# Kernel optimization log

Hardware: AMD Instinct MI355X
Metric: run time of the kernel (lower is better)

Reference implementation:

```python
import math
import jax, jax.numpy as jnp
import numpy as np

S = 4096          # total packed tokens (b*s with bsz=1)
NUM_HEADS = 16
HEAD_DIM = 80
SCALE = 1.0 / math.sqrt(HEAD_DIM)


def setup_inputs() -> dict:
    key = jax.random.key(0)
    kq, kk, kv = jax.random.split(key, 3)
    q = jax.random.normal(kq, (S, NUM_HEADS, HEAD_DIM), dtype=jnp.float32)
    k = jax.random.normal(kk, (S, NUM_HEADS, HEAD_DIM), dtype=jnp.float32)
    v = jax.random.normal(kv, (S, NUM_HEADS, HEAD_DIM), dtype=jnp.float32)
    # 4 packed sequences of 1024 tokens each (flatten_batch=True, bsz=1)
    cu_seqlens = jnp.array([0, 1024, 2048, 3072, 4096], dtype=jnp.int32)
    return {"q": q, "k": k, "v": v, "bsz": 1, "cu_seqlens": cu_seqlens}


def reference(q, k, v, bsz, cu_seqlens):
    # q/k/v: [(b s), h, d]; flatten_batch=True so bsz == 1
    s = q.shape[0] // bsz
    h, d = q.shape[1], q.shape[2]

    # Block-diagonal mask from cu_seqlens: True inside each packed sequence.
    seg = jnp.searchsorted(cu_seqlens[1:], jnp.arange(s), side="right")  # [s]
    mask = seg[:, None] == seg[None, :]                                  # [s, s]

    # '(b s) h d -> b h s d'
    qb = q.reshape(bsz, s, h, d).transpose(0, 2, 1, 3)
    kb = k.reshape(bsz, s, h, d).transpose(0, 2, 1, 3)
    vb = v.reshape(bsz, s, h, d).transpose(0, 2, 1, 3)

    scores = jnp.einsum("bhsd,bhtd->bhst", qb, kb) * SCALE
    bias = jnp.where(mask, jnp.zeros((), scores.dtype), jnp.finfo(scores.dtype).min)
    attn = jax.nn.softmax((scores + bias).astype(jnp.float32), axis=-1).astype(q.dtype)

    out = jnp.einsum("bhst,bhtd->bhsd", attn, vb)
    # 'b h s d -> (b s) h d'
    return out.transpose(0, 2, 1, 3).reshape(bsz * s, h, d)
```

## Files before the change

kernel.cpp:

```cpp
#include <hip/hip_runtime.h>
#include <hip/hip_bf16.h>
#include <math.h>

#define NTOK 4096
#define NH 16
#define HD 80
#define TOKSTRIDE (NH * HD)
#define QBLK 64
#define KVBLK 64
#define KSTR 80
#define VSTR 72
#define PSTR 72

typedef __bf16 bf16x4 __attribute__((ext_vector_type(4)));
typedef __bf16 bf16x8 __attribute__((ext_vector_type(8)));
typedef float  f32x4  __attribute__((ext_vector_type(4)));

__global__ __launch_bounds__(256)
void prepack(const float* __restrict__ qg, const float* __restrict__ kg,
             const float* __restrict__ vg, __bf16* __restrict__ qb,
             __bf16* __restrict__ kb, __bf16* __restrict__ vtb) {
  __shared__ __align__(16) __bf16 Vl[HD][VSTR];
  const int tid  = threadIdx.x;
  const int tok0 = blockIdx.x * 64;
  const int h    = blockIdx.y;
  const float qscale = 1.4426950408889634f / sqrtf((float)HD);

  for (int i = tid; i < 64 * 20; i += 256) {
    const int row = i / 20;
    const int c4  = (i % 20) * 4;
    const size_t gsrc = (size_t)(tok0 + row) * TOKSTRIDE + h * HD + c4;
    const size_t gdst = ((size_t)h * NTOK + tok0 + row) * HD + c4;

    float4 fq = *reinterpret_cast<const float4*>(qg + gsrc);
    bf16x4 uq;
    uq[0] = (__bf16)(fq.x * qscale); uq[1] = (__bf16)(fq.y * qscale);
    uq[2] = (__bf16)(fq.z * qscale); uq[3] = (__bf16)(fq.w * qscale);
    *reinterpret_cast<bf16x4*>(qb + gdst) = uq;

    float4 fk = *reinterpret_cast<const float4*>(kg + gsrc);
    bf16x4 uk;
    uk[0] = (__bf16)fk.x; uk[1] = (__bf16)fk.y;
    uk[2] = (__bf16)fk.z; uk[3] = (__bf16)fk.w;
    *reinterpret_cast<bf16x4*>(kb + gdst) = uk;

    float4 fv = *reinterpret_cast<const float4*>(vg + gsrc);
    Vl[c4 + 0][row] = (__bf16)fv.x; Vl[c4 + 1][row] = (__bf16)fv.y;
    Vl[c4 + 2][row] = (__bf16)fv.z; Vl[c4 + 3][row] = (__bf16)fv.w;
  }
  __syncthreads();
  for (int i = tid; i < HD * 8; i += 256) {
    const int d  = i / 8;
    const int c8 = (i % 8) * 8;
    bf16x8 val = *reinterpret_cast<const bf16x8*>(&Vl[d][c8]);
    *reinterpret_cast<bf16x8*>(vtb + ((size_t)h * HD + d) * NTOK + tok0 + c8) = val;
  }
}

__global__ __launch_bounds__(256, 4)
void vis_attn5(const __bf16* __restrict__ qb, const __bf16* __restrict__ kb,
               const __bf16* __restrict__ vtb, const int* __restrict__ cu,
               int n_cu, float* __restrict__ outg) {
  __shared__ __align__(16) __bf16 Kl[(KVBLK + 1) * KSTR];
  __shared__ __align__(16) __bf16 Vt[HD][VSTR];
  __shared__ __align__(16) __bf16 Pl[QBLK][PSTR];

  const int tid  = threadIdx.x;
  const int w    = tid >> 6;
  const int lane = tid & 63;
  const int lr   = lane & 15;
  const int g    = lane >> 4;

  const int q0 = blockIdx.x * QBLK;
  const int h  = blockIdx.y;

  int kv_start = 0, kv_end = NTOK;
  for (int i = 0; i + 1 < n_cu; ++i) {
    int a = cu[i], b = cu[i + 1];
    if (q0 >= a && q0 < b) { kv_start = a; kv_end = b; }
  }

  if (tid < 16) Kl[KVBLK * KSTR + tid] = (__bf16)0.0f;

  const int qrow = q0 + w * 16 + lr;
  const __bf16* qrptr = qb + ((size_t)h * NTOK + qrow) * HD;
  bf16x8 qf[3];
  #pragma unroll
  for (int c = 0; c < 3; ++c) {
    const int dbase = c * 32 + g * 8;
    if (dbase < HD) {
      qf[c] = *reinterpret_cast<const bf16x8*>(qrptr + dbase);
    } else {
      #pragma unroll
      for (int j = 0; j < 8; ++j) qf[c][j] = (__bf16)0.0f;
    }
  }

  bf16x8 vfl;
  {
    const __bf16 o = (lr == 0) ? (__bf16)1.0f : (__bf16)0.0f;
    #pragma unroll
    for (int j = 0; j < 8; ++j) vfl[j] = o;
  }

  f32x4 O[6];
  #pragma unroll
  for (int n = 0; n < 6; ++n) O[n] = (f32x4){0.f, 0.f, 0.f, 0.f};

  bf16x8 st[5];
  const __bf16* kbh  = kb  + (size_t)h * NTOK * HD;
  const __bf16* vtbh = vtb + (size_t)h * HD * NTOK;

  {
    const int kv0 = kv_start;
    #pragma unroll
    for (int j = 0; j < 5; ++j) {
      const int c = tid + j * 256;
      if (c < 640) {
        const int row = c / 10, col = (c % 10) * 8;
        st[j] = *reinterpret_cast<const bf16x8*>(kbh + (size_t)(kv0 + row) * HD + col);
      } else {
        const int c2 = c - 640, d = c2 / 8, kc = (c2 % 8) * 8;
        st[j] = *reinterpret_cast<const bf16x8*>(vtbh + (size_t)d * NTOK + kv0 + kc);
      }
    }
  }

  for (int kv0 = kv_start; kv0 < kv_end; kv0 += KVBLK) {
    __syncthreads();
    #pragma unroll
    for (int j = 0; j < 5; ++j) {
      const int c = tid + j * 256;
      if (c < 640) {
        const int row = c / 10, col = (c % 10) * 8;
        *reinterpret_cast<bf16x8*>(&Kl[row * KSTR + col]) = st[j];
      } else {
        const int c2 = c - 640, d = c2 / 8, kc = (c2 % 8) * 8;
        *reinterpret_cast<bf16x8*>(&Vt[d][kc]) = st[j];
      }
    }
    __syncthreads();

    if (kv0 + KVBLK < kv_end) {
      const int kvn = kv0 + KVBLK;
      #pragma unroll
      for (int j = 0; j < 5; ++j) {
        const int c = tid + j * 256;
        if (c < 640) {
          const int row = c / 10, col = (c % 10) * 8;
          st[j] = *reinterpret_cast<const bf16x8*>(kbh + (size_t)(kvn + row) * HD + col);
        } else {
          const int c2 = c - 640, d = c2 / 8, kc = (c2 % 8) * 8;
          st[j] = *reinterpret_cast<const bf16x8*>(vtbh + (size_t)d * NTOK + kvn + kc);
        }
      }
    }

    f32x4 S[4];
    __builtin_amdgcn_s_setprio(1);
    #pragma unroll
    for (int t = 0; t < 4; ++t) {
      S[t] = (f32x4){0.f, 0.f, 0.f, 0.f};
      #pragma unroll
      for (int c = 0; c < 3; ++c) {
        bf16x8 kf = *reinterpret_cast<const bf16x8*>(&Kl[(t * 16 + lr) * KSTR + c * 32 + g * 8]);
        S[t] = __builtin_amdgcn_mfma_f32_16x16x32_bf16(qf[c], kf, S[t], 0, 0, 0);
      }
    }
    __builtin_amdgcn_s_setprio(0);

    #pragma unroll
    for (int t = 0; t < 4; ++t) {
      #pragma unroll
      for (int r = 0; r < 4; ++r)
        S[t][r] = exp2f(S[t][r]);
    }

    #pragma unroll
    for (int t = 0; t < 4; ++t) {
      #pragma unroll
      for (int r = 0; r < 4; ++r)
        Pl[w * 16 + g * 4 + r][t * 16 + lr] = (__bf16)S[t][r];
    }

    #pragma unroll
    for (int kc = 0; kc < 2; ++kc) {
      bf16x8 pf = *reinterpret_cast<const bf16x8*>(&Pl[w * 16 + lr][kc * 32 + g * 8]);
      __builtin_amdgcn_s_setprio(1);
      #pragma unroll
      for (int n = 0; n < 5; ++n) {
        bf16x8 vf = *reinterpret_cast<const bf16x8*>(&Vt[n * 16 + lr][kc * 32 + g * 8]);
        O[n] = __builtin_amdgcn_mfma_f32_16x16x32_bf16(pf, vf, O[n], 0, 0, 0);
      }
      O[5] = __builtin_amdgcn_mfma_f32_16x16x32_bf16(pf, vfl, O[5], 0, 0, 0);
      __builtin_amdgcn_s_setprio(0);
    }
  }

  float inv[4];
  #pragma unroll
  for (int r = 0; r < 4; ++r) {
    float l = __shfl(O[5][r], lane & 48);
    inv[r] = 1.0f / l;
  }
  const int orow0 = q0 + w * 16 + g * 4;
  #pragma unroll
  for (int n = 0; n < 5; ++n) {
    #pragma unroll
    for (int r = 0; r < 4; ++r)
      outg[(size_t)(orow0 + r) * TOKSTRIDE + h * HD + n * 16 + lr] = O[n][r] * inv[r];
  }
}

__global__ __launch_bounds__(256, 4)
void vis_attn_fb(const float* __restrict__ qg, const float* __restrict__ kg,
                 const float* __restrict__ vg, const int* __restrict__ cu,
                 int n_cu, float* __restrict__ outg) {
  __shared__ __align__(16) __bf16 Kl[KVBLK][104];
  __shared__ __align__(16) __bf16 Vt[HD][72];
  __shared__ __align__(16) __bf16 Pl[64][72];

  const int tid  = threadIdx.x;
  const int w    = tid >> 6;
  const int lane = tid & 63;
  const int lr   = lane & 15;
  const int g    = lane >> 4;
  const int q0 = blockIdx.x * 64;
  const int h  = blockIdx.y;

  int kv_start = 0, kv_end = NTOK;
  for (int i = 0; i + 1 < n_cu; ++i) {
    int a = cu[i], b = cu[i + 1];
    if (q0 >= a && q0 < b) { kv_start = a; kv_end = b; }
  }
  for (int i = tid; i < KVBLK * 16; i += 256)
    Kl[i >> 4][HD + (i & 15)] = (__bf16)0.0f;

  const float qscale = 1.4426950408889634f / sqrtf((float)HD);
  const int qrow = q0 + w * 16 + lr;
  const float* qptr = qg + (size_t)qrow * TOKSTRIDE + h * HD;
  bf16x8 qf[3];
  #pragma unroll
  for (int c = 0; c < 3; ++c) {
    const int dbase = c * 32 + g * 8;
    if (dbase < HD) {
      float4 f0 = *reinterpret_cast<const float4*>(qptr + dbase);
      float4 f1 = *reinterpret_cast<const float4*>(qptr + dbase + 4);
      qf[c][0] = (__bf16)(f0.x * qscale); qf[c][1] = (__bf16)(f0.y * qscale);
      qf[c][2] = (__bf16)(f0.z * qscale); qf[c][3] = (__bf16)(f0.w * qscale);
      qf[c][4] = (__bf16)(f1.x * qscale); qf[c][5] = (__bf16)(f1.y * qscale);
      qf[c][6] = (__bf16)(f1.z * qscale); qf[c][7] = (__bf16)(f1.w * qscale);
    } else {
      #pragma unroll
      for (int j = 0; j < 8; ++j) qf[c][j] = (__bf16)0.0f;
    }
  }

  f32x4 O[5];
  #pragma unroll
  for (int n = 0; n < 5; ++n) O[n] = (f32x4){0.f, 0.f, 0.f, 0.f};
  float m_run[4] = {-1e30f, -1e30f, -1e30f, -1e30f};
  float l_run[4] = {0.f, 0.f, 0.f, 0.f};

  for (int kv0 = kv_start; kv0 < kv_end; kv0 += KVBLK) {
    __syncthreads();
    for (int i = tid; i < KVBLK * (HD / 4); i += 256) {
      const int row = i / (HD / 4);
      const int c4  = (i % (HD / 4)) * 4;
      float4 f = *reinterpret_cast<const float4*>(
          kg + (size_t)(kv0 + row) * TOKSTRIDE + h * HD + c4);
      Kl[row][c4 + 0] = (__bf16)f.x; Kl[row][c4 + 1] = (__bf16)f.y;
      Kl[row][c4 + 2] = (__bf16)f.z; Kl[row][c4 + 3] = (__bf16)f.w;
    }
    for (int i = tid; i < KVBLK * (HD / 4); i += 256) {
      const int row = i / (HD / 4);
      const int c4  = (i % (HD / 4)) * 4;
      float4 f = *reinterpret_cast<const float4*>(
          vg + (size_t)(kv0 + row) * TOKSTRIDE + h * HD + c4);
      Vt[c4 + 0][row] = (__bf16)f.x; Vt[c4 + 1][row] = (__bf16)f.y;
      Vt[c4 + 2][row] = (__bf16)f.z; Vt[c4 + 3][row] = (__bf16)f.w;
    }
    __syncthreads();

    f32x4 S[4];
    #pragma unroll
    for (int t = 0; t < 4; ++t) {
      S[t] = (f32x4){0.f, 0.f, 0.f, 0.f};
      #pragma unroll
      for (int c = 0; c < 3; ++c) {
        bf16x8 kf = *reinterpret_cast<const bf16x8*>(&Kl[t * 16 + lr][c * 32 + g * 8]);
        S[t] = __builtin_amdgcn_mfma_f32_16x16x32_bf16(qf[c], kf, S[t], 0, 0, 0);
      }
    }
    float pmax[4];
    #pragma unroll
    for (int r = 0; r < 4; ++r)
      pmax[r] = fmaxf(fmaxf(S[0][r], S[1][r]), fmaxf(S[2][r], S[3][r]));
    #pragma unroll
    for (int r = 0; r < 4; ++r) {
      pmax[r] = fmaxf(pmax[r], __shfl_xor(pmax[r], 1));
      pmax[r] = fmaxf(pmax[r], __shfl_xor(pmax[r], 2));
      pmax[r] = fmaxf(pmax[r], __shfl_xor(pmax[r], 4));
      pmax[r] = fmaxf(pmax[r], __shfl_xor(pmax[r], 8));
    }
    float alpha[4];
    #pragma unroll
    for (int r = 0; r < 4; ++r) {
      float mn = fmaxf(m_run[r], pmax[r]);
      alpha[r] = exp2f(m_run[r] - mn);
      m_run[r] = mn;
    }
    #pragma unroll
    for (int t = 0; t < 4; ++t) {
      #pragma unroll
      for (int r = 0; r < 4; ++r)
        S[t][r] = exp2f(S[t][r] - m_run[r]);
    }
    float rsum[4];
    #pragma unroll
    for (int r = 0; r < 4; ++r) {
      rsum[r] = (S[0][r] + S[1][r]) + (S[2][r] + S[3][r]);
      rsum[r] += __shfl_xor(rsum[r], 1);
      rsum[r] += __shfl_xor(rsum[r], 2);
      rsum[r] += __shfl_xor(rsum[r], 4);
      rsum[r] += __shfl_xor(rsum[r], 8);
      l_run[r] = l_run[r] * alpha[r] + rsum[r];
    }
    #pragma unroll
    for (int n = 0; n < 5; ++n) {
      #pragma unroll
      for (int r = 0; r < 4; ++r) O[n][r] *= alpha[r];
    }
    #pragma unroll
    for (int t = 0; t < 4; ++t) {
      #pragma unroll
      for (int r = 0; r < 4; ++r)
        Pl[w * 16 + g * 4 + r][t * 16 + lr] = (__bf16)S[t][r];
    }
    #pragma unroll
    for (int kc = 0; kc < 2; ++kc) {
      bf16x8 pf = *reinterpret_cast<const bf16x8*>(&Pl[w * 16 + lr][kc * 32 + g * 8]);
      #pragma unroll
      for (int n = 0; n < 5; ++n) {
        bf16x8 vf = *reinterpret_cast<const bf16x8*>(&Vt[n * 16 + lr][kc * 32 + g * 8]);
        O[n] = __builtin_amdgcn_mfma_f32_16x16x32_bf16(pf, vf, O[n], 0, 0, 0);
      }
    }
  }

  float inv[4];
  #pragma unroll
  for (int r = 0; r < 4; ++r) inv[r] = 1.0f / l_run[r];
  const int orow0 = q0 + w * 16 + g * 4;
  #pragma unroll
  for (int n = 0; n < 5; ++n) {
    #pragma unroll
    for (int r = 0; r < 4; ++r)
      outg[(size_t)(orow0 + r) * TOKSTRIDE + h * HD + n * 16 + lr] = O[n][r] * inv[r];
  }
}

extern "C" void kernel_launch(void* const* d_in, const int* in_sizes, int n_in,
                              void* d_out, int out_size, void* d_ws, size_t ws_size,
                              hipStream_t stream) {
  const float* q  = (const float*)d_in[0];
  const float* k  = (const float*)d_in[1];
  const float* v  = (const float*)d_in[2];
  const int* cu   = (const int*)d_in[4];
  const int n_cu  = in_sizes[4];
  float* out      = (float*)d_out;

  const size_t one = (size_t)NH * NTOK * HD * sizeof(__bf16);

  if (ws_size >= 3 * one) {
    __bf16* qb  = (__bf16*)d_ws;
    __bf16* kb  = (__bf16*)((char*)d_ws + one);
    __bf16* vtb = (__bf16*)((char*)d_ws + 2 * one);
    dim3 gp(NTOK / 64, NH);
    prepack<<<gp, 256, 0, stream>>>(q, k, v, qb, kb, vtb);
    dim3 ga(NTOK / QBLK, NH);
    vis_attn5<<<ga, 256, 0, stream>>>(qb, kb, vtb, cu, n_cu, out);
  } else {
    dim3 gf(NTOK / 64, NH);
    vis_attn_fb<<<gf, 256, 0, stream>>>(q, k, v, cu, n_cu, out);
  }
}
```

Baseline: 64.26 us.

## Split attention waves 2x2 over query rows and KV columns with LDS reduction

Reorganizes the four waves from one 16-row query strip each into a 2x2 grid: each wave handles 32 query rows against half of the 64-key block. Each K and V fragment read from LDS now feeds two MFMAs, which is meant to cut LDS read traffic per MFMA. Because each wave only sees half the keys, the partial O and row-sum accumulators are combined at the end through an LDS buffer that aliases the K/V/P shared memory. The price is extra registers for two query tiles and a final cross-wave reduction with additional barriers.

```diff
diff --git a/kernel.cpp b/kernel.cpp
--- a/kernel.cpp
+++ b/kernel.cpp
@@ -58,15 +58,19 @@
 }
 
 __global__ __launch_bounds__(256, 4)
-void vis_attn5(const __bf16* __restrict__ qb, const __bf16* __restrict__ kb,
+void vis_attn6(const __bf16* __restrict__ qb, const __bf16* __restrict__ kb,
                const __bf16* __restrict__ vtb, const int* __restrict__ cu,
                int n_cu, float* __restrict__ outg) {
-  __shared__ __align__(16) __bf16 Kl[(KVBLK + 1) * KSTR];
-  __shared__ __align__(16) __bf16 Vt[HD][VSTR];
-  __shared__ __align__(16) __bf16 Pl[QBLK][PSTR];
+  __shared__ __align__(16) unsigned char smem[31136];
+  __bf16* Kl = reinterpret_cast<__bf16*>(smem);
+  __bf16* Vt = reinterpret_cast<__bf16*>(smem + 10400);
+  __bf16* Pl = reinterpret_cast<__bf16*>(smem + 21920);
+  float*  Cx = reinterpret_cast<float*>(smem);
 
   const int tid  = threadIdx.x;
   const int w    = tid >> 6;
+  const int wr   = w >> 1;
+  const int wc   = w & 1;
   const int lane = tid & 63;
   const int lr   = lane & 15;
   const int g    = lane >> 4;
@@ -82,17 +86,20 @@
 
   if (tid < 16) Kl[KVBLK * KSTR + tid] = (__bf16)0.0f;
 
-  const int qrow = q0 + w * 16 + lr;
-  const __bf16* qrptr = qb + ((size_t)h * NTOK + qrow) * HD;
-  bf16x8 qf[3];
-  #pragma unroll
-  for (int c = 0; c < 3; ++c) {
-    const int dbase = c * 32 + g * 8;
-    if (dbase < HD) {
-      qf[c] = *reinterpret_cast<const bf16x8*>(qrptr + dbase);
-    } else {
-      #pragma unroll
-      for (int j = 0; j < 8; ++j) qf[c][j] = (__bf16)0.0f;
+  bf16x8 qf[2][3];
+  #pragma unroll
+  for (int m = 0; m < 2; ++m) {
+    const int qrow = q0 + wr * 32 + m * 16 + lr;
+    const __bf16* qrptr = qb + ((size_t)h * NTOK + qrow) * HD;
+    #pragma unroll
+    for (int c = 0; c < 3; ++c) {
+      const int dbase = c * 32 + g * 8;
+      if (dbase < HD) {
+        qf[m][c] = *reinterpret_cast<const bf16x8*>(qrptr + dbase);
+      } else {
+        #pragma unroll
+        for (int j = 0; j < 8; ++j) qf[m][c][j] = (__bf16)0.0f;
+      }
     }
   }
 
@@ -103,9 +110,14 @@
     for (int j = 0; j < 8; ++j) vfl[j] = o;
   }
 
-  f32x4 O[6];
-  #pragma unroll
-  for (int n = 0; n < 6; ++n) O[n] = (f32x4){0.f, 0.f, 0.f, 0.f};
+  f32x4 O[2][5];
+  f32x4 lacc[2];
+  #pragma unroll
+  for (int m = 0; m < 2; ++m) {
+    #pragma unroll
+    for (int n = 0; n < 5; ++n) O[m][n] = (f32x4){0.f, 0.f, 0.f, 0.f};
+    lacc[m] = (f32x4){0.f, 0.f, 0.f, 0.f};
+  }
 
   bf16x8 st[5];
   const __bf16* kbh  = kb  + (size_t)h * NTOK * HD;
@@ -136,7 +148,7 @@
         *reinterpret_cast<bf16x8*>(&Kl[row * KSTR + col]) = st[j];
       } else {
         const int c2 = c - 640, d = c2 / 8, kc = (c2 % 8) * 8;
-        *reinterpret_cast<bf16x8*>(&Vt[d][kc]) = st[j];
+        *reinterpret_cast<bf16x8*>(&Vt[d * VSTR + kc]) = st[j];
       }
     }
     __syncthreads();
@@ -156,59 +168,83 @@
       }
     }
 
-    f32x4 S[4];
-    __builtin_amdgcn_s_setprio(1);
-    #pragma unroll
-    for (int t = 0; t < 4; ++t) {
-      S[t] = (f32x4){0.f, 0.f, 0.f, 0.f};
-      #pragma unroll
-      for (int c = 0; c < 3; ++c) {
-        bf16x8 kf = *reinterpret_cast<const bf16x8*>(&Kl[(t * 16 + lr) * KSTR + c * 32 + g * 8]);
-        S[t] = __builtin_amdgcn_mfma_f32_16x16x32_bf16(qf[c], kf, S[t], 0, 0, 0);
-      }
-    }
-    __builtin_amdgcn_s_setprio(0);
-
-    #pragma unroll
-    for (int t = 0; t < 4; ++t) {
-      #pragma unroll
-      for (int r = 0; r < 4; ++r)
-        S[t][r] = exp2f(S[t][r]);
-    }
-
-    #pragma unroll
-    for (int t = 0; t < 4; ++t) {
-      #pragma unroll
-      for (int r = 0; r < 4; ++r)
-        Pl[w * 16 + g * 4 + r][t * 16 + lr] = (__bf16)S[t][r];
-    }
-
-    #pragma unroll
-    for (int kc = 0; kc < 2; ++kc) {
-      bf16x8 pf = *reinterpret_cast<const bf16x8*>(&Pl[w * 16 + lr][kc * 32 + g * 8]);
+    #pragma unroll
+    for (int m = 0; m < 2; ++m) {
+      f32x4 S[2];
       __builtin_amdgcn_s_setprio(1);
       #pragma unroll
+      for (int t = 0; t < 2; ++t) {
+        S[t] = (f32x4){0.f, 0.f, 0.f, 0.f};
+        #pragma unroll
+        for (int c = 0; c < 3; ++c) {
+          bf16x8 kf = *reinterpret_cast<const bf16x8*>(
+              &Kl[(wc * 32 + t * 16 + lr) * KSTR + c * 32 + g * 8]);
+          S[t] = __builtin_amdgcn_mfma_f32_16x16x32_bf16(qf[m][c], kf, S[t], 0, 0, 0);
+        }
+      }
+      __builtin_amdgcn_s_setprio(0);
+      #pragma unroll
+      for (int t = 0; t < 2; ++t) {
+        #pragma unroll
+        for (int r = 0; r < 4; ++r)
+          Pl[(wr * 32 + m * 16 + g * 4 + r) * PSTR + wc * 32 + t * 16 + lr] =
+              (__bf16)exp2f(S[t][r]);
+      }
+    }
+
+    #pragma unroll
+    for (int m = 0; m < 2; ++m) {
+      bf16x8 pf = *reinterpret_cast<const bf16x8*>(
+          &Pl[(wr * 32 + m * 16 + lr) * PSTR + wc * 32 + g * 8]);
+      __builtin_amdgcn_s_setprio(1);
+      #pragma unroll
       for (int n = 0; n < 5; ++n) {
-        bf16x8 vf = *reinterpret_cast<const bf16x8*>(&Vt[n * 16 + lr][kc * 32 + g * 8]);
-        O[n] = __builtin_amdgcn_mfma_f32_16x16x32_bf16(pf, vf, O[n], 0, 0, 0);
-      }
-      O[5] = __builtin_amdgcn_mfma_f32_16x16x32_bf16(pf, vfl, O[5], 0, 0, 0);
+        bf16x8 vf = *reinterpret_cast<const bf16x8*>(
+            &Vt[(n * 16 + lr) * VSTR + wc * 32 + g * 8]);
+        O[m][n] = __builtin_amdgcn_mfma_f32_16x16x32_bf16(pf, vf, O[m][n], 0, 0, 0);
+      }
+      lacc[m] = __builtin_amdgcn_mfma_f32_16x16x32_bf16(pf, vfl, lacc[m], 0, 0, 0);
       __builtin_amdgcn_s_setprio(0);
     }
   }
 
-  float inv[4];
-  #pragma unroll
-  for (int r = 0; r < 4; ++r) {
-    float l = __shfl(O[5][r], lane & 48);
-    inv[r] = 1.0f / l;
-  }
-  const int orow0 = q0 + w * 16 + g * 4;
-  #pragma unroll
-  for (int n = 0; n < 5; ++n) {
-    #pragma unroll
-    for (int r = 0; r < 4; ++r)
-      outg[(size_t)(orow0 + r) * TOKSTRIDE + h * HD + n * 16 + lr] = O[n][r] * inv[r];
+  __syncthreads();
+  if (wc == 1) {
+    #pragma unroll
+    for (int m = 0; m < 2; ++m) {
+      #pragma unroll
+      for (int n = 0; n < 6; ++n) {
+        f32x4 v = (n < 5) ? O[m][n] : lacc[m];
+        *reinterpret_cast<f32x4*>(&Cx[((wr * 12 + m * 6 + n) * 64 + lane) * 4]) = v;
+      }
+    }
+  }
+  __syncthreads();
+  if (wc == 0) {
+    #pragma unroll
+    for (int m = 0; m < 2; ++m) {
+      #pragma unroll
+      for (int n = 0; n < 5; ++n) {
+        f32x4 p = *reinterpret_cast<const f32x4*>(&Cx[((wr * 12 + m * 6 + n) * 64 + lane) * 4]);
+        O[m][n] += p;
+      }
+      f32x4 lp = *reinterpret_cast<const f32x4*>(&Cx[((wr * 12 + m * 6 + 5) * 64 + lane) * 4]);
+      lacc[m] += lp;
+
+      float inv[4];
+      #pragma unroll
+      for (int r = 0; r < 4; ++r) {
+        float l = __shfl(lacc[m][r], lane & 48);
+        inv[r] = 1.0f / l;
+      }
+      const int orow0 = q0 + wr * 32 + m * 16 + g * 4;
+      #pragma unroll
+      for (int n = 0; n < 5; ++n) {
+        #pragma unroll
+        for (int r = 0; r < 4; ++r)
+          outg[(size_t)(orow0 + r) * TOKSTRIDE + h * HD + n * 16 + lr] = O[m][n][r] * inv[r];
+      }
+    }
   }
 }
 
@@ -379,7 +415,7 @@
     dim3 gp(NTOK / 64, NH);
     prepack<<<gp, 256, 0, stream>>>(q, k, v, qb, kb, vtb);
     dim3 ga(NTOK / QBLK, NH);
-    vis_attn5<<<ga, 256, 0, stream>>>(qb, kb, vtb, cu, n_cu, out);
+    vis_attn6<<<ga, 256, 0, stream>>>(qb, kb, vtb, cu, n_cu, out);
   } else {
     dim3 gf(NTOK / 64, NH);
     vis_attn_fb<<<gf, 256, 0, stream>>>(q, k, v, cu, n_cu, out);
```

New measurement: 118.9 us. 85.1% more time.
